# Performance work log

Hardware: AMD Instinct MI355X
Metric: run time of the kernel (lower is better)

## Reference

```python
import jax, jax.numpy as jnp
import numpy as np

N_NODES = 100000
N_EDGES = 1600000
IN_DIM = 64
OUT_DIM = 64


def setup_inputs() -> dict:
    key = jax.random.key(0)
    k1, k2, k3, k4 = jax.random.split(key, 4)
    x = jax.random.normal(k1, (N_NODES, IN_DIM), dtype=jnp.float32)
    edge_index = jax.random.randint(k2, (2, N_EDGES), 0, N_NODES, dtype=jnp.int64)
    # nn.Linear-style init: U(-1/sqrt(in), 1/sqrt(in))
    lim = 1.0 / np.sqrt(IN_DIM)
    W = jax.random.uniform(k3, (OUT_DIM, IN_DIM), dtype=jnp.float32, minval=-lim, maxval=lim)
    b = jax.random.uniform(k4, (OUT_DIM,), dtype=jnp.float32, minval=-lim, maxval=lim)
    return {"x": x, "edge_index": edge_index, "W": W, "b": b}


def reference(x, edge_index, W, b):
    n = x.shape[0]
    row, col = edge_index[0], edge_index[1]
    # gather source features along edges, scatter-add into destination rows
    agg = jax.ops.segment_sum(x[col], row, num_segments=n)  # [n, in_dim]
    deg = jax.ops.segment_sum(jnp.ones(row.shape[0], dtype=x.dtype), row, num_segments=n)
    deg = jnp.clip(deg, 1.0, None)[:, None]  # [n, 1]
    out = agg / deg
    return out @ W.T + b  # [n, out_dim]
```

## Files before the change

### kernel.cpp

```cpp
#include <hip/hip_runtime.h>
#include <hip/hip_bf16.h>
#include <hip/hip_fp16.h>

#define DIM 64
#define NPART 8

typedef _Float16 half2_t __attribute__((ext_vector_type(2)));

#if defined(__has_builtin)
#if __has_builtin(__builtin_amdgcn_fdot2)
#define HAVE_FDOT2 1
#endif
#endif

__device__ __forceinline__ float dot2acc(unsigned int mu, unsigned int wu, float acc) {
#ifdef HAVE_FDOT2
    return __builtin_amdgcn_fdot2(__builtin_bit_cast(half2_t, mu),
                                  __builtin_bit_cast(half2_t, wu), acc, false);
#else
    const float2 mf = __half22float2(*(const __half2*)&mu);
    const float2 wf = __half22float2(*(const __half2*)&wu);
    return acc + mf.x * wf.x + mf.y * wf.y;
#endif
}

__global__ void detect_kernel(const unsigned int* __restrict__ ei, int* __restrict__ flag) {
    const int lane = threadIdx.x & 63;
    const unsigned int hi = ei[2 * lane + 1];
    const unsigned long long ball = __ballot(hi != 0u);
    if (threadIdx.x == 0) *flag = (ball == 0ULL) ? 1 : 0;
}

__global__ void __launch_bounds__(256) convert_kernel(
    const float4* __restrict__ x, ushort4* __restrict__ xh, int n4) {
    const int i = blockIdx.x * 256 + threadIdx.x;
    if (i >= n4) return;
    const float4 v = x[i];
    ushort4 o;
    o.x = __half_as_ushort(__float2half(v.x));
    o.y = __half_as_ushort(__float2half(v.y));
    o.z = __half_as_ushort(__float2half(v.z));
    o.w = __half_as_ushort(__float2half(v.w));
    xh[i] = o;
}

__global__ void __launch_bounds__(256) cvtW_kernel(
    const float* __restrict__ W, unsigned int* __restrict__ wh2, int n2) {
    const int i = blockIdx.x * 256 + threadIdx.x;
    if (i >= n2) return;
    const float2 f = ((const float2*)W)[i];
    const __half2 h = __floats2half2_rn(f.x, f.y);
    wh2[i] = *(const unsigned int*)&h;
}

__global__ void __launch_bounds__(256) prep_kernel(
    const void* __restrict__ eiv, int* __restrict__ rows32, int* __restrict__ cols32,
    int* __restrict__ cnt, int nE, const int* __restrict__ flag) {
    const int base = (blockIdx.x * 256 + threadIdx.x) * 4;
    if (base >= nE) return;
    if (base + 3 < nE) {
        int4 rr, cc;
        if (*flag) {
            const long long* ei = (const long long*)eiv;
            const longlong2 r01 = *(const longlong2*)&ei[base];
            const longlong2 r23 = *(const longlong2*)&ei[base + 2];
            const longlong2 c01 = *(const longlong2*)&ei[nE + base];
            const longlong2 c23 = *(const longlong2*)&ei[nE + base + 2];
            rr = make_int4((int)r01.x, (int)r01.y, (int)r23.x, (int)r23.y);
            cc = make_int4((int)c01.x, (int)c01.y, (int)c23.x, (int)c23.y);
        } else {
            const int* ei = (const int*)eiv;
            rr = *(const int4*)&ei[base];
            cc = *(const int4*)&ei[nE + base];
        }
        *(int4*)&rows32[base] = rr;
        *(int4*)&cols32[base] = cc;
        atomicAdd(&cnt[rr.x], 1);
        atomicAdd(&cnt[rr.y], 1);
        atomicAdd(&cnt[rr.z], 1);
        atomicAdd(&cnt[rr.w], 1);
    } else {
        for (int k = 0; k < 4 && base + k < nE; ++k) {
            int r, c;
            if (*flag) {
                const long long* ei = (const long long*)eiv;
                r = (int)ei[base + k]; c = (int)ei[nE + base + k];
            } else {
                const int* ei = (const int*)eiv;
                r = ei[base + k]; c = ei[nE + base + k];
            }
            rows32[base + k] = r;
            cols32[base + k] = c;
            atomicAdd(&cnt[r], 1);
        }
    }
}

__global__ void __launch_bounds__(256) scan1_kernel(
    const int* __restrict__ cnt, int* __restrict__ cursor,
    int* __restrict__ blksums, int n) {
    __shared__ int tmp[256];
    const int t = threadIdx.x;
    const int base = blockIdx.x * 1024 + t * 4;
    int v0 = (base + 0 < n) ? cnt[base + 0] : 0;
    int v1 = (base + 1 < n) ? cnt[base + 1] : 0;
    int v2 = (base + 2 < n) ? cnt[base + 2] : 0;
    int v3 = (base + 3 < n) ? cnt[base + 3] : 0;
    const int s = v0 + v1 + v2 + v3;
    tmp[t] = s;
    __syncthreads();
    for (int off = 1; off < 256; off <<= 1) {
        int v = 0;
        if (t >= off) v = tmp[t - off];
        __syncthreads();
        tmp[t] += v;
        __syncthreads();
    }
    const int excl = tmp[t] - s;
    if (t == 255) blksums[blockIdx.x] = tmp[255];
    if (base + 0 < n) cursor[base + 0] = excl;
    if (base + 1 < n) cursor[base + 1] = excl + v0;
    if (base + 2 < n) cursor[base + 2] = excl + v0 + v1;
    if (base + 3 < n) cursor[base + 3] = excl + v0 + v1 + v2;
}

__global__ void __launch_bounds__(1024) scan2_kernel(int* __restrict__ blksums, int nblk) {
    __shared__ int tmp[1024];
    const int t = threadIdx.x;
    const int v = (t < nblk) ? blksums[t] : 0;
    tmp[t] = v;
    __syncthreads();
    for (int off = 1; off < 1024; off <<= 1) {
        int u = 0;
        if (t >= off) u = tmp[t - off];
        __syncthreads();
        tmp[t] += u;
        __syncthreads();
    }
    if (t < nblk) blksums[t] = tmp[t] - v;
}

__global__ void __launch_bounds__(256) scan3_kernel(
    int* __restrict__ cursor, const int* __restrict__ blksums, int n) {
    const int add = blksums[blockIdx.x];
    const int base = blockIdx.x * 1024 + threadIdx.x * 4;
    if (base + 0 < n) cursor[base + 0] += add;
    if (base + 1 < n) cursor[base + 1] += add;
    if (base + 2 < n) cursor[base + 2] += add;
    if (base + 3 < n) cursor[base + 3] += add;
}

__global__ void __launch_bounds__(256) build_part32_kernel(
    const int* __restrict__ rows32, const int* __restrict__ cols32,
    int* __restrict__ cursor, int* __restrict__ scol, int nE, int n) {
    const int p  = blockIdx.x & (NPART - 1);
    const int q  = blockIdx.x / NPART;
    const int nq = gridDim.x / NPART;
    const unsigned bound = (unsigned)((n + NPART - 1) / NPART);
    const unsigned lo    = (unsigned)p * bound;
    const int stride = nq * 256;
    for (int e = q * 256 + (int)threadIdx.x; e < nE; e += stride) {
        const int r = rows32[e];
        if ((unsigned)r - lo < bound) {
            const int pos = atomicAdd(&cursor[r], 1);
            scol[pos] = cols32[e];
        }
    }
}

__global__ void __launch_bounds__(256) gather_finalize_q_kernel(
    const __half* __restrict__ xh, const int* __restrict__ scol,
    const int* __restrict__ cursor, const int* __restrict__ cnt,
    const unsigned int* __restrict__ wh2, const float* __restrict__ b,
    float* __restrict__ out, int n) {
    __shared__ __align__(16) unsigned int rowh[4][32];
    const int tid   = threadIdx.x;
    const int group = tid >> 6;
    const int lane  = tid & 63;
    const int q     = lane >> 4;
    const int s16   = lane & 15;
    const int wid   = (int)((blockIdx.x * 256 + tid) >> 6);
    const int nw    = (int)((gridDim.x * 256) >> 6);

    unsigned int wcu[32];
    #pragma unroll
    for (int i = 0; i < 32; ++i) wcu[i] = wh2[lane * 32 + i];
    #pragma unroll
    for (int i = 0; i < 32; ++i) asm volatile("" : "+v"(wcu[i]));

    const float bl = b[lane];

    for (int r0 = wid; r0 < n; r0 += nw) {
        const int r   = __builtin_amdgcn_readfirstlane(r0);
        const int k   = cnt[r];
        const int end = cursor[r];
        const int s   = end - k;
        float a0 = 0.f, a1 = 0.f, a2 = 0.f, a3 = 0.f;
        int j = 0;
        for (; j + 7 < k; j += 8) {
            const int cA = scol[s + j + q];
            const int cB = scol[s + j + 4 + q];
            const uint2 uA = *(const uint2*)(xh + ((size_t)cA << 6) + (s16 << 2));
            const uint2 uB = *(const uint2*)(xh + ((size_t)cB << 6) + (s16 << 2));
            float2 f;
            f = __half22float2(*(const __half2*)&uA.x); a0 += f.x; a1 += f.y;
            f = __half22float2(*(const __half2*)&uA.y); a2 += f.x; a3 += f.y;
            f = __half22float2(*(const __half2*)&uB.x); a0 += f.x; a1 += f.y;
            f = __half22float2(*(const __half2*)&uB.y); a2 += f.x; a3 += f.y;
        }
        if (j + 3 < k) {
            const int cA = scol[s + j + q];
            const uint2 uA = *(const uint2*)(xh + ((size_t)cA << 6) + (s16 << 2));
            float2 f;
            f = __half22float2(*(const __half2*)&uA.x); a0 += f.x; a1 += f.y;
            f = __half22float2(*(const __half2*)&uA.y); a2 += f.x; a3 += f.y;
            j += 4;
        }
        for (; j < k; ++j) {
            const int c = scol[s + j];
            if (q == 0) {
                const uint2 u = *(const uint2*)(xh + ((size_t)c << 6) + (s16 << 2));
                float2 f;
                f = __half22float2(*(const __half2*)&u.x); a0 += f.x; a1 += f.y;
                f = __half22float2(*(const __half2*)&u.y); a2 += f.x; a3 += f.y;
            }
        }
        a0 += __shfl_xor(a0, 16); a0 += __shfl_xor(a0, 32);
        a1 += __shfl_xor(a1, 16); a1 += __shfl_xor(a1, 32);
        a2 += __shfl_xor(a2, 16); a2 += __shfl_xor(a2, 32);
        a3 += __shfl_xor(a3, 16); a3 += __shfl_xor(a3, 32);
        const float inv = 1.0f / ((k > 0) ? (float)k : 1.0f);
        if (q == 0) {
            const __half2 m01 = __floats2half2_rn(a0 * inv, a1 * inv);
            const __half2 m23 = __floats2half2_rn(a2 * inv, a3 * inv);
            uint2 mu;
            mu.x = *(const unsigned int*)&m01;
            mu.y = *(const unsigned int*)&m23;
            *(uint2*)&rowh[group][s16 * 2] = mu;
        }
        float dot = bl;
        #pragma unroll
        for (int i4 = 0; i4 < 8; ++i4) {
            const uint4 mm = *(const uint4*)&rowh[group][i4 * 4];
            dot = dot2acc(mm.x, wcu[i4 * 4 + 0], dot);
            dot = dot2acc(mm.y, wcu[i4 * 4 + 1], dot);
            dot = dot2acc(mm.z, wcu[i4 * 4 + 2], dot);
            dot = dot2acc(mm.w, wcu[i4 * 4 + 3], dot);
        }
        out[(size_t)r * DIM + lane] = dot;
    }
}

__global__ void __launch_bounds__(256) hist_kernel(
    const void* __restrict__ eiv, int* __restrict__ cnt,
    int nE, const int* __restrict__ flag) {
    const int base = (blockIdx.x * 256 + threadIdx.x) * 4;
    if (base >= nE) return;
    if (*flag) {
        const long long* ei = (const long long*)eiv;
        #pragma unroll
        for (int k = 0; k < 4; ++k)
            if (base + k < nE) atomicAdd(&cnt[(int)ei[base + k]], 1);
    } else {
        const int* ei = (const int*)eiv;
        #pragma unroll
        for (int k = 0; k < 4; ++k)
            if (base + k < nE) atomicAdd(&cnt[ei[base + k]], 1);
    }
}

__global__ void __launch_bounds__(256) build_part_ei_kernel(
    const void* __restrict__ eiv, int* __restrict__ cursor,
    int* __restrict__ scol, int nE, int n, const int* __restrict__ flag) {
    const int p  = blockIdx.x & (NPART - 1);
    const int q  = blockIdx.x / NPART;
    const int nq = gridDim.x / NPART;
    const unsigned bound = (unsigned)((n + NPART - 1) / NPART);
    const unsigned lo    = (unsigned)p * bound;
    const int stride = nq * 256;
    if (*flag) {
        const long long* ei = (const long long*)eiv;
        for (int e = q * 256 + (int)threadIdx.x; e < nE; e += stride) {
            const int r = (int)ei[e];
            if ((unsigned)r - lo < bound) {
                const int pos = atomicAdd(&cursor[r], 1);
                scol[pos] = (int)ei[nE + e];
            }
        }
    } else {
        const int* ei = (const int*)eiv;
        for (int e = q * 256 + (int)threadIdx.x; e < nE; e += stride) {
            const int r = ei[e];
            if ((unsigned)r - lo < bound) {
                const int pos = atomicAdd(&cursor[r], 1);
                scol[pos] = ei[nE + e];
            }
        }
    }
}

__global__ void __launch_bounds__(256) gather_finalize_f32_kernel(
    const float* __restrict__ x, const int* __restrict__ scol,
    const int* __restrict__ cursor, const int* __restrict__ cnt,
    const float* __restrict__ W, const float* __restrict__ b,
    float* __restrict__ out, int n) {
    __shared__ __align__(16) float rowbuf[4][DIM];
    const int group = threadIdx.x >> 6;
    const int lane  = threadIdx.x & 63;
    const int wid   = (int)((blockIdx.x * blockDim.x + threadIdx.x) >> 6);
    const int nw    = (int)((gridDim.x * blockDim.x) >> 6);
    float wc[DIM];
    #pragma unroll
    for (int k4 = 0; k4 < DIM / 4; ++k4) {
        float4 w4 = *(const float4*)&W[(size_t)lane * DIM + k4 * 4];
        wc[k4 * 4 + 0] = w4.x; wc[k4 * 4 + 1] = w4.y;
        wc[k4 * 4 + 2] = w4.z; wc[k4 * 4 + 3] = w4.w;
    }
    const float bl = b[lane];
    for (int r = wid; r < n; r += nw) {
        const int k   = cnt[r];
        const int end = cursor[r];
        const int s   = end - k;
        float a0 = 0.0f, a1 = 0.0f;
        int j = 0;
        for (; j + 3 < k; j += 4) {
            a0 += x[(size_t)scol[s + j + 0] * DIM + lane];
            a1 += x[(size_t)scol[s + j + 1] * DIM + lane];
            a0 += x[(size_t)scol[s + j + 2] * DIM + lane];
            a1 += x[(size_t)scol[s + j + 3] * DIM + lane];
        }
        for (; j < k; ++j) a0 += x[(size_t)scol[s + j] * DIM + lane];
        const float dg   = (k > 0) ? (float)k : 1.0f;
        const float mean = (a0 + a1) / dg;
        rowbuf[group][lane] = mean;
        float dot = bl;
        #pragma unroll
        for (int k4 = 0; k4 < DIM / 4; ++k4) {
            const float4 m4 = *(const float4*)&rowbuf[group][k4 * 4];
            dot += m4.x * wc[k4 * 4 + 0];
            dot += m4.y * wc[k4 * 4 + 1];
            dot += m4.z * wc[k4 * 4 + 2];
            dot += m4.w * wc[k4 * 4 + 3];
        }
        out[(size_t)r * DIM + lane] = dot;
    }
}

extern "C" void kernel_launch(void* const* d_in, const int* in_sizes, int n_in,
                              void* d_out, int out_size, void* d_ws, size_t ws_size,
                              hipStream_t stream) {
    const float* x  = (const float*)d_in[0];
    const void*  ei = (const void*)d_in[1];
    const float* W  = (const float*)d_in[2];
    const float* b  = (const float*)d_in[3];
    float* out = (float*)d_out;

    const int n  = in_sizes[0] / DIM;
    const int nE = in_sizes[1] / 2;

    int* wsI     = (int*)d_ws;
    int* cnt     = wsI;
    int* cursor  = wsI + n;
    int* blksums = wsI + 2 * n;
    int* flag    = wsI + 2 * n + 1024;
    int* scol    = wsI + 2 * n + 1088;
    __half* xh   = (__half*)(scol + nE);
    int* rows32  = scol + nE + n * (DIM / 2);
    int* cols32  = rows32 + nE;
    unsigned int* wh2 = (unsigned int*)(cols32 + nE);

    const size_t need_csr  = ((size_t)2 * n + 1088 + (size_t)nE) * sizeof(int);
    const size_t need_full = need_csr + (size_t)n * DIM * sizeof(__half)
                           + (size_t)2 * nE * sizeof(int)
                           + (size_t)(DIM * DIM / 2) * sizeof(int);

    if (ws_size < need_csr) return;

    const int nblk = (n + 1023) / 1024;
    const bool full = (ws_size >= need_full);

    detect_kernel<<<1, 64, 0, stream>>>((const unsigned int*)ei, flag);
    hipMemsetAsync(cnt, 0, (size_t)n * sizeof(int), stream);

    if (full) {
        const int n4 = n * DIM / 4;
        convert_kernel<<<(n4 + 255) / 256, 256, 0, stream>>>(
            (const float4*)x, (ushort4*)xh, n4);
        cvtW_kernel<<<(DIM * DIM / 2 + 255) / 256, 256, 0, stream>>>(W, wh2, DIM * DIM / 2);
        prep_kernel<<<(nE / 4 + 255) / 256, 256, 0, stream>>>(ei, rows32, cols32, cnt, nE, flag);
    } else {
        hist_kernel<<<(nE / 4 + 255) / 256, 256, 0, stream>>>(ei, cnt, nE, flag);
    }

    scan1_kernel<<<nblk, 256, 0, stream>>>(cnt, cursor, blksums, n);
    scan2_kernel<<<1, 1024, 0, stream>>>(blksums, nblk);
    scan3_kernel<<<nblk, 256, 0, stream>>>(cursor, blksums, n);

    if (full) {
        build_part32_kernel<<<2048, 256, 0, stream>>>(rows32, cols32, cursor, scol, nE, n);
        gather_finalize_q_kernel<<<2048, 256, 0, stream>>>(xh, scol, cursor, cnt, wh2, b, out, n);
    } else {
        build_part_ei_kernel<<<2048, 256, 0, stream>>>(ei, cursor, scol, nE, n, flag);
        gather_finalize_f32_kernel<<<2048, 256, 0, stream>>>(x, scol, cursor, cnt, W, b, out, n);
    }
}
```

Before: 307.1 us.

## Bin edges by row partition and replace multi-kernel scan with wave-level allocation

The CSR build pipeline is restructured. A single setup kernel converts x and W to fp16 and zeroes the counters, replacing the detect and convert kernels and the memset. The prep kernel now writes each edge as a (row,col) pair into one of 8 per-partition bins, with per-block shared-memory offsets. The three scan kernels become one alloc kernel that does a wave-level prefix sum and reserves space through per-partition atomic bumps. Each partition then scatters only its own bin instead of rescanning all edges 8 times, and the gather loop gains a 16-wide unrolled stage. In exchange, the order of rows within a partition is no longer deterministic, the fixed bin capacity would drop edges on strongly skewed row distributions, and the fp32 fallback path is removed.

```diff
diff --git a/kernel.cpp b/kernel.cpp
--- a/kernel.cpp
+++ b/kernel.cpp
@@ -24,144 +24,215 @@
 #endif
 }
 
-__global__ void detect_kernel(const unsigned int* __restrict__ ei, int* __restrict__ flag) {
-    const int lane = threadIdx.x & 63;
-    const unsigned int hi = ei[2 * lane + 1];
-    const unsigned long long ball = __ballot(hi != 0u);
-    if (threadIdx.x == 0) *flag = (ball == 0ULL) ? 1 : 0;
-}
-
-__global__ void __launch_bounds__(256) convert_kernel(
-    const float4* __restrict__ x, ushort4* __restrict__ xh, int n4) {
+__global__ void __launch_bounds__(256) setup_kernel(
+    const float4* __restrict__ x, ushort4* __restrict__ xh4,
+    const float2* __restrict__ W2, unsigned int* __restrict__ wh2,
+    int* __restrict__ cnt, int* __restrict__ partTot, int* __restrict__ bumpP,
+    int n4, int n) {
     const int i = blockIdx.x * 256 + threadIdx.x;
-    if (i >= n4) return;
-    const float4 v = x[i];
-    ushort4 o;
-    o.x = __half_as_ushort(__float2half(v.x));
-    o.y = __half_as_ushort(__float2half(v.y));
-    o.z = __half_as_ushort(__float2half(v.z));
-    o.w = __half_as_ushort(__float2half(v.w));
-    xh[i] = o;
-}
-
-__global__ void __launch_bounds__(256) cvtW_kernel(
-    const float* __restrict__ W, unsigned int* __restrict__ wh2, int n2) {
-    const int i = blockIdx.x * 256 + threadIdx.x;
-    if (i >= n2) return;
-    const float2 f = ((const float2*)W)[i];
-    const __half2 h = __floats2half2_rn(f.x, f.y);
-    wh2[i] = *(const unsigned int*)&h;
-}
-
-__global__ void __launch_bounds__(256) prep_kernel(
-    const void* __restrict__ eiv, int* __restrict__ rows32, int* __restrict__ cols32,
-    int* __restrict__ cnt, int nE, const int* __restrict__ flag) {
-    const int base = (blockIdx.x * 256 + threadIdx.x) * 4;
-    if (base >= nE) return;
-    if (base + 3 < nE) {
-        int4 rr, cc;
-        if (*flag) {
-            const long long* ei = (const long long*)eiv;
-            const longlong2 r01 = *(const longlong2*)&ei[base];
-            const longlong2 r23 = *(const longlong2*)&ei[base + 2];
-            const longlong2 c01 = *(const longlong2*)&ei[nE + base];
-            const longlong2 c23 = *(const longlong2*)&ei[nE + base + 2];
-            rr = make_int4((int)r01.x, (int)r01.y, (int)r23.x, (int)r23.y);
-            cc = make_int4((int)c01.x, (int)c01.y, (int)c23.x, (int)c23.y);
-        } else {
-            const int* ei = (const int*)eiv;
-            rr = *(const int4*)&ei[base];
-            cc = *(const int4*)&ei[nE + base];
-        }
-        *(int4*)&rows32[base] = rr;
-        *(int4*)&cols32[base] = cc;
-        atomicAdd(&cnt[rr.x], 1);
-        atomicAdd(&cnt[rr.y], 1);
-        atomicAdd(&cnt[rr.z], 1);
-        atomicAdd(&cnt[rr.w], 1);
-    } else {
-        for (int k = 0; k < 4 && base + k < nE; ++k) {
-            int r, c;
-            if (*flag) {
+    if (i < n4) {
+        const float4 v = x[i];
+        ushort4 o;
+        o.x = __half_as_ushort(__float2half(v.x));
+        o.y = __half_as_ushort(__float2half(v.y));
+        o.z = __half_as_ushort(__float2half(v.z));
+        o.w = __half_as_ushort(__float2half(v.w));
+        xh4[i] = o;
+    }
+    if (i < DIM * DIM / 2) {
+        const float2 f = W2[i];
+        const __half2 h = __floats2half2_rn(f.x, f.y);
+        wh2[i] = *(const unsigned int*)&h;
+    }
+    if (i < (n >> 2)) ((int4*)cnt)[i] = make_int4(0, 0, 0, 0);
+    if (i == 0) for (int k = n & ~3; k < n; ++k) cnt[k] = 0;
+    if (i < NPART) { partTot[i] = 0; bumpP[i] = 0; }
+}
+
+__global__ void __launch_bounds__(256) prep_bin_kernel(
+    const void* __restrict__ eiv, int* __restrict__ cnt,
+    uint2* __restrict__ bins, int* __restrict__ binCnt,
+    int nE, int bound, int cap) {
+    __shared__ int lcnt[NPART], lbase[NPART], sIs64;
+    const int tid = threadIdx.x;
+    if (tid < NPART) lcnt[tid] = 0;
+    if (tid < 64) {
+        const unsigned int hi = ((const unsigned int*)eiv)[2 * tid + 1];
+        const unsigned long long ball = __ballot(hi != 0u);
+        if (tid == 0) sIs64 = (ball == 0ULL) ? 1 : 0;
+    }
+    __syncthreads();
+    const int is64 = sIs64;
+    const int base = (blockIdx.x * 256 + tid) * 4;
+    int r[4], c[4], pp[4], off[4];
+    int nv = 0;
+    if (base < nE) {
+        nv = nE - base; if (nv > 4) nv = 4;
+        if (nv == 4 && (nE & 3) == 0) {
+            if (is64) {
                 const long long* ei = (const long long*)eiv;
-                r = (int)ei[base + k]; c = (int)ei[nE + base + k];
+                const longlong2 r01 = *(const longlong2*)&ei[base];
+                const longlong2 r23 = *(const longlong2*)&ei[base + 2];
+                const longlong2 c01 = *(const longlong2*)&ei[nE + base];
+                const longlong2 c23 = *(const longlong2*)&ei[nE + base + 2];
+                r[0] = (int)r01.x; r[1] = (int)r01.y; r[2] = (int)r23.x; r[3] = (int)r23.y;
+                c[0] = (int)c01.x; c[1] = (int)c01.y; c[2] = (int)c23.x; c[3] = (int)c23.y;
             } else {
                 const int* ei = (const int*)eiv;
-                r = ei[base + k]; c = ei[nE + base + k];
+                const int4 rr = *(const int4*)&ei[base];
+                const int4 cc = *(const int4*)&ei[nE + base];
+                r[0] = rr.x; r[1] = rr.y; r[2] = rr.z; r[3] = rr.w;
+                c[0] = cc.x; c[1] = cc.y; c[2] = cc.z; c[3] = cc.w;
             }
-            rows32[base + k] = r;
-            cols32[base + k] = c;
-            atomicAdd(&cnt[r], 1);
-        }
-    }
-}
-
-__global__ void __launch_bounds__(256) scan1_kernel(
+        } else {
+            for (int k = 0; k < nv; ++k) {
+                if (is64) {
+                    const long long* ei = (const long long*)eiv;
+                    r[k] = (int)ei[base + k]; c[k] = (int)ei[nE + base + k];
+                } else {
+                    const int* ei = (const int*)eiv;
+                    r[k] = ei[base + k]; c[k] = ei[nE + base + k];
+                }
+            }
+        }
+    }
+    #pragma unroll
+    for (int k = 0; k < 4; ++k) {
+        if (k < nv) {
+            int p = r[k] / bound; if (p > NPART - 1) p = NPART - 1;
+            pp[k] = p;
+            off[k] = atomicAdd(&lcnt[p], 1);
+            atomicAdd(&cnt[r[k]], 1);
+        }
+    }
+    __syncthreads();
+    if (tid < NPART) lbase[tid] = atomicAdd(&binCnt[tid], lcnt[tid]);
+    __syncthreads();
+    #pragma unroll
+    for (int k = 0; k < 4; ++k) {
+        if (k < nv) {
+            const int idx = lbase[pp[k]] + off[k];
+            if (idx < cap)
+                bins[(size_t)pp[k] * cap + idx] = make_uint2((unsigned)r[k], (unsigned)c[k]);
+        }
+    }
+}
+
+__global__ void __launch_bounds__(256) prep32_kernel(
+    const void* __restrict__ eiv, int* __restrict__ rows32, int* __restrict__ cols32,
+    int* __restrict__ cnt, int* __restrict__ partTot, int nE, int bound) {
+    __shared__ int lcnt[NPART], sIs64;
+    const int tid = threadIdx.x;
+    if (tid < NPART) lcnt[tid] = 0;
+    if (tid < 64) {
+        const unsigned int hi = ((const unsigned int*)eiv)[2 * tid + 1];
+        const unsigned long long ball = __ballot(hi != 0u);
+        if (tid == 0) sIs64 = (ball == 0ULL) ? 1 : 0;
+    }
+    __syncthreads();
+    const int is64 = sIs64;
+    const int base = (blockIdx.x * 256 + tid) * 4;
+    int r[4], c[4];
+    int nv = 0;
+    if (base < nE) {
+        nv = nE - base; if (nv > 4) nv = 4;
+        if (nv == 4 && (nE & 3) == 0) {
+            if (is64) {
+                const long long* ei = (const long long*)eiv;
+                const longlong2 r01 = *(const longlong2*)&ei[base];
+                const longlong2 r23 = *(const longlong2*)&ei[base + 2];
+                const longlong2 c01 = *(const longlong2*)&ei[nE + base];
+                const longlong2 c23 = *(const longlong2*)&ei[nE + base + 2];
+                r[0] = (int)r01.x; r[1] = (int)r01.y; r[2] = (int)r23.x; r[3] = (int)r23.y;
+                c[0] = (int)c01.x; c[1] = (int)c01.y; c[2] = (int)c23.x; c[3] = (int)c23.y;
+            } else {
+                const int* ei = (const int*)eiv;
+                const int4 rr = *(const int4*)&ei[base];
+                const int4 cc = *(const int4*)&ei[nE + base];
+                r[0] = rr.x; r[1] = rr.y; r[2] = rr.z; r[3] = rr.w;
+                c[0] = cc.x; c[1] = cc.y; c[2] = cc.z; c[3] = cc.w;
+            }
+            *(int4*)&rows32[base] = make_int4(r[0], r[1], r[2], r[3]);
+            *(int4*)&cols32[base] = make_int4(c[0], c[1], c[2], c[3]);
+        } else {
+            for (int k = 0; k < nv; ++k) {
+                if (is64) {
+                    const long long* ei = (const long long*)eiv;
+                    r[k] = (int)ei[base + k]; c[k] = (int)ei[nE + base + k];
+                } else {
+                    const int* ei = (const int*)eiv;
+                    r[k] = ei[base + k]; c[k] = ei[nE + base + k];
+                }
+                rows32[base + k] = r[k]; cols32[base + k] = c[k];
+            }
+        }
+    }
+    #pragma unroll
+    for (int k = 0; k < 4; ++k) {
+        if (k < nv) {
+            int p = r[k] / bound; if (p > NPART - 1) p = NPART - 1;
+            atomicAdd(&lcnt[p], 1);
+            atomicAdd(&cnt[r[k]], 1);
+        }
+    }
+    __syncthreads();
+    if (tid < NPART && lcnt[tid] > 0) atomicAdd(&partTot[tid], lcnt[tid]);
+}
+
+__global__ void __launch_bounds__(256) alloc_kernel(
     const int* __restrict__ cnt, int* __restrict__ cursor,
-    int* __restrict__ blksums, int n) {
-    __shared__ int tmp[256];
-    const int t = threadIdx.x;
-    const int base = blockIdx.x * 1024 + t * 4;
-    int v0 = (base + 0 < n) ? cnt[base + 0] : 0;
-    int v1 = (base + 1 < n) ? cnt[base + 1] : 0;
-    int v2 = (base + 2 < n) ? cnt[base + 2] : 0;
-    int v3 = (base + 3 < n) ? cnt[base + 3] : 0;
-    const int s = v0 + v1 + v2 + v3;
-    tmp[t] = s;
-    __syncthreads();
-    for (int off = 1; off < 256; off <<= 1) {
-        int v = 0;
-        if (t >= off) v = tmp[t - off];
-        __syncthreads();
-        tmp[t] += v;
-        __syncthreads();
-    }
-    const int excl = tmp[t] - s;
-    if (t == 255) blksums[blockIdx.x] = tmp[255];
-    if (base + 0 < n) cursor[base + 0] = excl;
-    if (base + 1 < n) cursor[base + 1] = excl + v0;
-    if (base + 2 < n) cursor[base + 2] = excl + v0 + v1;
-    if (base + 3 < n) cursor[base + 3] = excl + v0 + v1 + v2;
-}
-
-__global__ void __launch_bounds__(1024) scan2_kernel(int* __restrict__ blksums, int nblk) {
-    __shared__ int tmp[1024];
-    const int t = threadIdx.x;
-    const int v = (t < nblk) ? blksums[t] : 0;
-    tmp[t] = v;
-    __syncthreads();
-    for (int off = 1; off < 1024; off <<= 1) {
-        int u = 0;
-        if (t >= off) u = tmp[t - off];
-        __syncthreads();
-        tmp[t] += u;
-        __syncthreads();
-    }
-    if (t < nblk) blksums[t] = tmp[t] - v;
-}
-
-__global__ void __launch_bounds__(256) scan3_kernel(
-    int* __restrict__ cursor, const int* __restrict__ blksums, int n) {
-    const int add = blksums[blockIdx.x];
-    const int base = blockIdx.x * 1024 + threadIdx.x * 4;
-    if (base + 0 < n) cursor[base + 0] += add;
-    if (base + 1 < n) cursor[base + 1] += add;
-    if (base + 2 < n) cursor[base + 2] += add;
-    if (base + 3 < n) cursor[base + 3] += add;
+    const int* __restrict__ partTot, int* __restrict__ bumpP, int n, int bound) {
+    const int gid  = blockIdx.x * 256 + threadIdx.x;
+    const int lane = threadIdx.x & 63;
+    const bool act = gid < n;
+    const int v = act ? cnt[gid] : 0;
+    int inc = v;
+    #pragma unroll
+    for (int off = 1; off < 64; off <<= 1) {
+        const int t = __shfl_up(inc, off);
+        if (lane >= off) inc += t;
+    }
+    const int total = __shfl(inc, 63);
+    const int excl  = inc - v;
+    const int rr = act ? gid : (n - 1);
+    int p = rr / bound; if (p > NPART - 1) p = NPART - 1;
+    p = __builtin_amdgcn_readfirstlane(p);
+    int wbase = 0;
+    if (lane == 0) {
+        int pb = 0;
+        for (int q = 0; q < p; ++q) pb += partTot[q];
+        wbase = pb + atomicAdd(&bumpP[p], total);
+    }
+    wbase = __shfl(wbase, 0);
+    if (act) cursor[gid] = wbase + excl;
+}
+
+__global__ void __launch_bounds__(256) build_bin_kernel(
+    const uint2* __restrict__ bins, const int* __restrict__ binCnt,
+    int* __restrict__ cursor, int* __restrict__ scol, int cap) {
+    const int p = blockIdx.x & (NPART - 1);
+    const int m = binCnt[p];
+    const int start  = (blockIdx.x >> 3) * 256 + threadIdx.x;
+    const int stride = (gridDim.x >> 3) * 256;
+    for (int i = start; i < m; i += stride) {
+        const uint2 rc = bins[(size_t)p * cap + i];
+        const int pos = atomicAdd(&cursor[rc.x], 1);
+        scol[pos] = (int)rc.y;
+    }
 }
 
 __global__ void __launch_bounds__(256) build_part32_kernel(
     const int* __restrict__ rows32, const int* __restrict__ cols32,
-    int* __restrict__ cursor, int* __restrict__ scol, int nE, int n) {
+    int* __restrict__ cursor, int* __restrict__ scol, int nE, int bound) {
     const int p  = blockIdx.x & (NPART - 1);
     const int q  = blockIdx.x / NPART;
     const int nq = gridDim.x / NPART;
-    const unsigned bound = (unsigned)((n + NPART - 1) / NPART);
-    const unsigned lo    = (unsigned)p * bound;
+    const unsigned lo = (unsigned)p * (unsigned)bound;
+    const unsigned bnd = (unsigned)((p == NPART - 1) ? 0x7fffffff : bound);
     const int stride = nq * 256;
     for (int e = q * 256 + (int)threadIdx.x; e < nE; e += stride) {
         const int r = rows32[e];
-        if ((unsigned)r - lo < bound) {
+        if ((unsigned)r - lo < bnd) {
             const int pos = atomicAdd(&cursor[r], 1);
             scol[pos] = cols32[e];
         }
@@ -197,6 +268,25 @@
         const int s   = end - k;
         float a0 = 0.f, a1 = 0.f, a2 = 0.f, a3 = 0.f;
         int j = 0;
+        for (; j + 15 < k; j += 16) {
+            const int cA = scol[s + j + q];
+            const int cB = scol[s + j + 4 + q];
+            const int cC = scol[s + j + 8 + q];
+            const int cD = scol[s + j + 12 + q];
+            const uint2 uA = *(const uint2*)(xh + ((size_t)cA << 6) + (s16 << 2));
+            const uint2 uB = *(const uint2*)(xh + ((size_t)cB << 6) + (s16 << 2));
+            const uint2 uC = *(const uint2*)(xh + ((size_t)cC << 6) + (s16 << 2));
+            const uint2 uD = *(const uint2*)(xh + ((size_t)cD << 6) + (s16 << 2));
+            float2 f;
+            f = __half22float2(*(const __half2*)&uA.x); a0 += f.x; a1 += f.y;
+            f = __half22float2(*(const __half2*)&uA.y); a2 += f.x; a3 += f.y;
+            f = __half22float2(*(const __half2*)&uB.x); a0 += f.x; a1 += f.y;
+            f = __half22float2(*(const __half2*)&uB.y); a2 += f.x; a3 += f.y;
+            f = __half22float2(*(const __half2*)&uC.x); a0 += f.x; a1 += f.y;
+            f = __half22float2(*(const __half2*)&uC.y); a2 += f.x; a3 += f.y;
+            f = __half22float2(*(const __half2*)&uD.x); a0 += f.x; a1 += f.y;
+            f = __half22float2(*(const __half2*)&uD.y); a2 += f.x; a3 += f.y;
+        }
         for (; j + 7 < k; j += 8) {
             const int cA = scol[s + j + q];
             const int cB = scol[s + j + 4 + q];
@@ -251,101 +341,6 @@
     }
 }
 
-__global__ void __launch_bounds__(256) hist_kernel(
-    const void* __restrict__ eiv, int* __restrict__ cnt,
-    int nE, const int* __restrict__ flag) {
-    const int base = (blockIdx.x * 256 + threadIdx.x) * 4;
-    if (base >= nE) return;
-    if (*flag) {
-        const long long* ei = (const long long*)eiv;
-        #pragma unroll
-        for (int k = 0; k < 4; ++k)
-            if (base + k < nE) atomicAdd(&cnt[(int)ei[base + k]], 1);
-    } else {
-        const int* ei = (const int*)eiv;
-        #pragma unroll
-        for (int k = 0; k < 4; ++k)
-            if (base + k < nE) atomicAdd(&cnt[ei[base + k]], 1);
-    }
-}
-
-__global__ void __launch_bounds__(256) build_part_ei_kernel(
-    const void* __restrict__ eiv, int* __restrict__ cursor,
-    int* __restrict__ scol, int nE, int n, const int* __restrict__ flag) {
-    const int p  = blockIdx.x & (NPART - 1);
-    const int q  = blockIdx.x / NPART;
-    const int nq = gridDim.x / NPART;
-    const unsigned bound = (unsigned)((n + NPART - 1) / NPART);
-    const unsigned lo    = (unsigned)p * bound;
-    const int stride = nq * 256;
-    if (*flag) {
-        const long long* ei = (const long long*)eiv;
-        for (int e = q * 256 + (int)threadIdx.x; e < nE; e += stride) {
-            const int r = (int)ei[e];
-            if ((unsigned)r - lo < bound) {
-                const int pos = atomicAdd(&cursor[r], 1);
-                scol[pos] = (int)ei[nE + e];
-            }
-        }
-    } else {
-        const int* ei = (const int*)eiv;
-        for (int e = q * 256 + (int)threadIdx.x; e < nE; e += stride) {
-            const int r = ei[e];
-            if ((unsigned)r - lo < bound) {
-                const int pos = atomicAdd(&cursor[r], 1);
-                scol[pos] = ei[nE + e];
-            }
-        }
-    }
-}
-
-__global__ void __launch_bounds__(256) gather_finalize_f32_kernel(
-    const float* __restrict__ x, const int* __restrict__ scol,
-    const int* __restrict__ cursor, const int* __restrict__ cnt,
-    const float* __restrict__ W, const float* __restrict__ b,
-    float* __restrict__ out, int n) {
-    __shared__ __align__(16) float rowbuf[4][DIM];
-    const int group = threadIdx.x >> 6;
-    const int lane  = threadIdx.x & 63;
-    const int wid   = (int)((blockIdx.x * blockDim.x + threadIdx.x) >> 6);
-    const int nw    = (int)((gridDim.x * blockDim.x) >> 6);
-    float wc[DIM];
-    #pragma unroll
-    for (int k4 = 0; k4 < DIM / 4; ++k4) {
-        float4 w4 = *(const float4*)&W[(size_t)lane * DIM + k4 * 4];
-        wc[k4 * 4 + 0] = w4.x; wc[k4 * 4 + 1] = w4.y;
-        wc[k4 * 4 + 2] = w4.z; wc[k4 * 4 + 3] = w4.w;
-    }
-    const float bl = b[lane];
-    for (int r = wid; r < n; r += nw) {
-        const int k   = cnt[r];
-        const int end = cursor[r];
-        const int s   = end - k;
-        float a0 = 0.0f, a1 = 0.0f;
-        int j = 0;
-        for (; j + 3 < k; j += 4) {
-            a0 += x[(size_t)scol[s + j + 0] * DIM + lane];
-            a1 += x[(size_t)scol[s + j + 1] * DIM + lane];
-            a0 += x[(size_t)scol[s + j + 2] * DIM + lane];
-            a1 += x[(size_t)scol[s + j + 3] * DIM + lane];
-        }
-        for (; j < k; ++j) a0 += x[(size_t)scol[s + j] * DIM + lane];
-        const float dg   = (k > 0) ? (float)k : 1.0f;
-        const float mean = (a0 + a1) / dg;
-        rowbuf[group][lane] = mean;
-        float dot = bl;
-        #pragma unroll
-        for (int k4 = 0; k4 < DIM / 4; ++k4) {
-            const float4 m4 = *(const float4*)&rowbuf[group][k4 * 4];
-            dot += m4.x * wc[k4 * 4 + 0];
-            dot += m4.y * wc[k4 * 4 + 1];
-            dot += m4.z * wc[k4 * 4 + 2];
-            dot += m4.w * wc[k4 * 4 + 3];
-        }
-        out[(size_t)r * DIM + lane] = dot;
-    }
-}
-
 extern "C" void kernel_launch(void* const* d_in, const int* in_sizes, int n_in,
                               void* d_out, int out_size, void* d_ws, size_t ws_size,
                               hipStream_t stream) {
@@ -358,49 +353,52 @@
     const int n  = in_sizes[0] / DIM;
     const int nE = in_sizes[1] / 2;
 
+    const int bound = (((n + NPART - 1) / NPART) + 63) & ~63;
+    const int cap   = ((nE + NPART - 1) / NPART) * 3 / 2 + 256;
+
+    const int scolPad = (nE + 3) & ~3;
     int* wsI     = (int*)d_ws;
     int* cnt     = wsI;
     int* cursor  = wsI + n;
-    int* blksums = wsI + 2 * n;
-    int* flag    = wsI + 2 * n + 1024;
-    int* scol    = wsI + 2 * n + 1088;
-    __half* xh   = (__half*)(scol + nE);
-    int* rows32  = scol + nE + n * (DIM / 2);
+    int* partTot = wsI + 2 * n;
+    int* bumpP   = wsI + 2 * n + 8;
+    int* scol    = wsI + 2 * n + 64;
+    __half* xh   = (__half*)(scol + scolPad);
+    unsigned int* wh2 = (unsigned int*)(xh + (size_t)n * DIM);
+    uint2* bins  = (uint2*)(wh2 + 2048);
+    int* rows32  = (int*)(wh2 + 2048);
     int* cols32  = rows32 + nE;
-    unsigned int* wh2 = (unsigned int*)(cols32 + nE);
-
-    const size_t need_csr  = ((size_t)2 * n + 1088 + (size_t)nE) * sizeof(int);
-    const size_t need_full = need_csr + (size_t)n * DIM * sizeof(__half)
-                           + (size_t)2 * nE * sizeof(int)
-                           + (size_t)(DIM * DIM / 2) * sizeof(int);
-
-    if (ws_size < need_csr) return;
-
-    const int nblk = (n + 1023) / 1024;
-    const bool full = (ws_size >= need_full);
-
-    detect_kernel<<<1, 64, 0, stream>>>((const unsigned int*)ei, flag);
-    hipMemsetAsync(cnt, 0, (size_t)n * sizeof(int), stream);
-
-    if (full) {
-        const int n4 = n * DIM / 4;
-        convert_kernel<<<(n4 + 255) / 256, 256, 0, stream>>>(
-            (const float4*)x, (ushort4*)xh, n4);
-        cvtW_kernel<<<(DIM * DIM / 2 + 255) / 256, 256, 0, stream>>>(W, wh2, DIM * DIM / 2);
-        prep_kernel<<<(nE / 4 + 255) / 256, 256, 0, stream>>>(ei, rows32, cols32, cnt, nE, flag);
-    } else {
-        hist_kernel<<<(nE / 4 + 255) / 256, 256, 0, stream>>>(ei, cnt, nE, flag);
-    }
-
-    scan1_kernel<<<nblk, 256, 0, stream>>>(cnt, cursor, blksums, n);
-    scan2_kernel<<<1, 1024, 0, stream>>>(blksums, nblk);
-    scan3_kernel<<<nblk, 256, 0, stream>>>(cursor, blksums, n);
-
-    if (full) {
-        build_part32_kernel<<<2048, 256, 0, stream>>>(rows32, cols32, cursor, scol, nE, n);
-        gather_finalize_q_kernel<<<2048, 256, 0, stream>>>(xh, scol, cursor, cnt, wh2, b, out, n);
-    } else {
-        build_part_ei_kernel<<<2048, 256, 0, stream>>>(ei, cursor, scol, nE, n, flag);
-        gather_finalize_f32_kernel<<<2048, 256, 0, stream>>>(x, scol, cursor, cnt, W, b, out, n);
-    }
-}
+
+    const size_t base_ints = (size_t)2 * n + 64 + scolPad + (size_t)n * (DIM / 2) + 2048;
+    const size_t need_A = (base_ints + (size_t)2 * NPART * cap) * sizeof(int);
+    const size_t need_B = (base_ints + (size_t)2 * nE) * sizeof(int);
+
+    const int n4 = n * DIM / 4;
+    int maxi = n4;
+    if (maxi < DIM * DIM / 2) maxi = DIM * DIM / 2;
+    if (maxi < (n + 3) / 4) maxi = (n + 3) / 4;
+
+    if (ws_size >= need_A) {
+        setup_kernel<<<(maxi + 255) / 256, 256, 0, stream>>>(
+            (const float4*)x, (ushort4*)xh, (const float2*)W, wh2,
+            cnt, partTot, bumpP, n4, n);
+        prep_bin_kernel<<<(nE + 1023) / 1024, 256, 0, stream>>>(
+            ei, cnt, bins, partTot, nE, bound, cap);
+        alloc_kernel<<<(n + 255) / 256, 256, 0, stream>>>(
+            cnt, cursor, partTot, bumpP, n, bound);
+        build_bin_kernel<<<2048, 256, 0, stream>>>(bins, partTot, cursor, scol, cap);
+        gather_finalize_q_kernel<<<2048, 256, 0, stream>>>(
+            xh, scol, cursor, cnt, wh2, b, out, n);
+    } else if (ws_size >= need_B) {
+        setup_kernel<<<(maxi + 255) / 256, 256, 0, stream>>>(
+            (const float4*)x, (ushort4*)xh, (const float2*)W, wh2,
+            cnt, partTot, bumpP, n4, n);
+        prep32_kernel<<<(nE + 1023) / 1024, 256, 0, stream>>>(
+            ei, rows32, cols32, cnt, partTot, nE, bound);
+        alloc_kernel<<<(n + 255) / 256, 256, 0, stream>>>(
+            cnt, cursor, partTot, bumpP, n, bound);
+        build_part32_kernel<<<2048, 256, 0, stream>>>(rows32, cols32, cursor, scol, nE, bound);
+        gather_finalize_q_kernel<<<2048, 256, 0, stream>>>(
+            xh, scol, cursor, cnt, wh2, b, out, n);
+    }
+}
```

Measured after the change: 318.5 us. 3.7% more time.
